# Kernel tuning notes

Measured on AMD Instinct MI355X. Metric: run time of the kernel, lower is better.

## Reference

```python
import jax, jax.numpy as jnp
import numpy as np
from jax import lax

NUM_HEADS = 4
EPS = 1e-12  # torch F.normalize eps


def _conv1x1(x, w):
    # x: [b, cin, h, w], w: [cout, cin] -> [b, cout, h, w]
    return jnp.einsum('bchw,oc->bohw', x, w)


def _dwconv3x3(x, w):
    # depthwise 3x3, padding=1; w: [C, 1, 3, 3]
    return lax.conv_general_dilated(
        x, w, window_strides=(1, 1), padding='SAME',
        feature_group_count=x.shape[1],
        dimension_numbers=('NCHW', 'OIHW', 'NCHW'))


def _l2norm(x):
    # F.normalize over last dim
    n = jnp.linalg.norm(x, axis=-1, keepdims=True)
    return x / jnp.maximum(n, EPS)


def _mdta(q, k, v, temperature, h, w):
    # q,k,v: [b, C, h, w] -> channel attention per head -> [b, C, h, w]
    b, c, _, _ = q.shape
    ch = c // NUM_HEADS
    def to_heads(t):
        return t.reshape(b, NUM_HEADS, ch, h * w)  # b head c (hw)
    qh, kh, vh = to_heads(q), to_heads(k), to_heads(v)
    qh = _l2norm(qh)
    kh = _l2norm(kh)
    attn = jnp.einsum('bhcn,bhdn->bhcd', qh, kh) * temperature  # [b,head,ch,ch]
    attn = jax.nn.softmax(attn, axis=-1)
    out = jnp.einsum('bhcd,bhdn->bhcn', attn, vh)
    return out.reshape(b, c, h, w)


def setup_inputs() -> dict:
    key = jax.random.key(0)
    ks = jax.random.split(key, 7)
    b, c, h, w = 2, 192, 128, 128
    return {
        'x': jax.random.normal(ks[0], (b, c, h, w), jnp.float32),
        'y': jax.random.normal(ks[1], (b, c, h, w), jnp.float32),
        'qkv_w': jax.random.normal(ks[2], (3 * c, c), jnp.float32) * (1.0 / np.sqrt(c)),
        'dw_w': jax.random.normal(ks[3], (3 * c, 1, 3, 3), jnp.float32) * (1.0 / 3.0),
        'kv_w': jax.random.normal(ks[4], (2 * c, c), jnp.float32) * (1.0 / np.sqrt(c)),
        'proj_w': jax.random.normal(ks[5], (c, c), jnp.float32) * (1.0 / np.sqrt(c)),
        'temperature': jnp.ones((NUM_HEADS, 1, 1), jnp.float32),
    }


def reference(x, y, qkv_w, dw_w, kv_w, proj_w, temperature):
    b, c, h, w = x.shape
    qkv = _dwconv3x3(_conv1x1(x, qkv_w), dw_w)
    q, k, v = jnp.split(qkv, 3, axis=1)
    # intra_fusion_attention(q, y): kv from y, channel attention with q
    kv = _conv1x1(y, kv_w)
    k2, v2 = jnp.split(kv, 2, axis=1)
    q = _mdta(q, k2, v2, temperature, h, w)
    out = _mdta(q, k, v, temperature, h, w)
    return _conv1x1(out, proj_w)
```

## Files before the change

### kernel.cpp

```cpp
#include <hip/hip_runtime.h>
#include <hip/hip_bf16.h>

#define HW 16384
#define IMGW 128
#define Bsz 2
#define Cc 192
#define NH 4
#define CH 48
static const size_t CP = (size_t)Cc * HW;

typedef __attribute__((ext_vector_type(4))) float f32x4;
typedef __attribute__((ext_vector_type(8))) short short8;
typedef __attribute__((ext_vector_type(8))) unsigned short bf16x8;
typedef __attribute__((ext_vector_type(4))) unsigned short bf16x4;

__device__ __forceinline__ unsigned short f2bf(float f) {
  __hip_bfloat16 h = __float2bfloat16(f);
  return *reinterpret_cast<unsigned short*>(&h);
}
__device__ __forceinline__ float bf2f(unsigned short u) {
  union { unsigned int i; float f; } v;
  v.i = (unsigned int)u << 16;
  return v.f;
}

#define NWQKV (576 * 192)
#define NWKV  (384 * 192)
__global__ __launch_bounds__(256) void cast_weights_kernel(
    const float* __restrict__ qkv_w, const float* __restrict__ kv_w,
    unsigned short* __restrict__ wqkv, unsigned short* __restrict__ wkv) {
  int i = blockIdx.x * 256 + threadIdx.x;
  if (i < NWQKV) wqkv[i] = f2bf(qkv_w[i]);
  else if (i < NWQKV + NWKV) wkv[i - NWQKV] = f2bf(kv_w[i - NWQKV]);
}

__global__ __launch_bounds__(256) void cast_xy_kernel(
    const float* __restrict__ x, const float* __restrict__ y,
    unsigned short* __restrict__ xt, unsigned short* __restrict__ yt) {
  const int z = blockIdx.z;
  const int b = z & 1;
  const float* in = (z >> 1) ? y : x;
  unsigned short* outt = (z >> 1) ? yt : xt;
  const int c0 = blockIdx.y * 8;
  const int hw = blockIdx.x * 256 + threadIdx.x;
  const float* ib = in + (size_t)b * CP;
  bf16x8 u;
  #pragma unroll
  for (int j = 0; j < 8; ++j)
    u[j] = f2bf(ib[(size_t)(c0 + j) * HW + hw]);
  *(bf16x8*)&outt[(size_t)b * CP + (size_t)hw * Cc + c0] = u;
}

#define BMH 128
#define BNO 64
#define BKC 64
#define PADK 72

template <int OUTBF16>
__global__ __launch_bounds__(256) void conv_mfma_kernel(
    const unsigned short* __restrict__ xt,
    const unsigned short* __restrict__ wb,
    void* __restrict__ outv, int Cout, size_t wstride) {
  __shared__ __align__(16) short As[BMH * PADK];
  __shared__ __align__(16) short Bs[BNO * PADK];
  const int b = blockIdx.z;
  const int hw0 = blockIdx.x * BMH;
  const int o0 = blockIdx.y * BNO;
  const int tid = threadIdx.x;
  const int lane = tid & 63, wid = tid >> 6;
  const int wm = wid & 1, wn = wid >> 1;
  const unsigned short* xtb = xt + (size_t)b * CP + (size_t)hw0 * Cc;
  const unsigned short* wbb = wb + (size_t)b * wstride + (size_t)o0 * Cc;
  f32x4 acc[4][2] = {};
  for (int k0 = 0; k0 < Cc; k0 += BKC) {
    #pragma unroll
    for (int p = 0; p < 4; ++p) {
      int i = tid + p * 256;
      int row = i >> 3, cc = i & 7;
      *(short8*)&As[row * PADK + cc * 8] =
          *(const short8*)(xtb + (size_t)row * Cc + k0 + cc * 8);
    }
    #pragma unroll
    for (int p = 0; p < 2; ++p) {
      int i = tid + p * 256;
      int row = i >> 3, cc = i & 7;
      *(short8*)&Bs[row * PADK + cc * 8] =
          *(const short8*)(wbb + (size_t)row * Cc + k0 + cc * 8);
    }
    __syncthreads();
    #pragma unroll
    for (int ks = 0; ks < 2; ++ks) {
      short8 bfrag[2];
      #pragma unroll
      for (int fn = 0; fn < 2; ++fn)
        bfrag[fn] = *(short8*)&Bs[(wn * 32 + fn * 16 + (lane & 15)) * PADK +
                                  ks * 32 + (lane >> 4) * 8];
      #pragma unroll
      for (int fm = 0; fm < 4; ++fm) {
        short8 afrag = *(short8*)&As[(wm * 64 + fm * 16 + (lane & 15)) * PADK +
                                     ks * 32 + (lane >> 4) * 8];
        #pragma unroll
        for (int fn = 0; fn < 2; ++fn)
          acc[fm][fn] = __builtin_amdgcn_mfma_f32_16x16x32_bf16(
              afrag, bfrag[fn], acc[fm][fn], 0, 0, 0);
      }
    }
    __syncthreads();
  }
  #pragma unroll
  for (int fm = 0; fm < 4; ++fm)
    #pragma unroll
    for (int fn = 0; fn < 2; ++fn) {
      int o = o0 + wn * 32 + fn * 16 + (lane & 15);
      int hw = hw0 + wm * 64 + fm * 16 + ((lane >> 4) << 2);
      if (OUTBF16) {
        bf16x4 u;
        #pragma unroll
        for (int r = 0; r < 4; ++r) u[r] = f2bf(acc[fm][fn][r]);
        *(bf16x4*)&((unsigned short*)outv)[((size_t)b * Cout + o) * HW + hw] = u;
      } else {
        *(f32x4*)&((float*)outv)[((size_t)b * Cout + o) * HW + hw] = acc[fm][fn];
      }
    }
}

__global__ __launch_bounds__(256) void dwconv_kernel(
    const unsigned short* __restrict__ in, const float* __restrict__ wgt,
    unsigned short* __restrict__ out, int Ctot) {
  const int b = blockIdx.z, ch = blockIdx.y;
  const int p0 = blockIdx.x * 2048 + threadIdx.x * 8;
  const int y = p0 >> 7, x0 = p0 & 127;
  const unsigned short* ip = in + ((size_t)b * Ctot + ch) * HW;
  const float* wp = wgt + ch * 9;
  float acc[8] = {};
  #pragma unroll
  for (int dy = -1; dy <= 1; ++dy) {
    int yy = y + dy;
    if (yy < 0 || yy > IMGW - 1) continue;
    const unsigned short* rp = ip + yy * IMGW;
    float r[10];
    bf16x8 mid = *(const bf16x8*)&rp[x0];
    #pragma unroll
    for (int e = 0; e < 8; ++e) r[e + 1] = bf2f(mid[e]);
    r[0] = (x0 > 0) ? bf2f(rp[x0 - 1]) : 0.f;
    r[9] = (x0 < 120) ? bf2f(rp[x0 + 8]) : 0.f;
    #pragma unroll
    for (int dx = 0; dx < 3; ++dx) {
      float wv = wp[(dy + 1) * 3 + dx];
      #pragma unroll
      for (int e = 0; e < 8; ++e) acc[e] += wv * r[e + dx];
    }
  }
  bf16x8 u;
  #pragma unroll
  for (int e = 0; e < 8; ++e) u[e] = f2bf(acc[e]);
  *(bf16x8*)&out[((size_t)b * Ctot + ch) * HW + p0] = u;
}

__global__ __launch_bounds__(256) void norm3_kernel(
    const unsigned short* __restrict__ qkvb,
    const unsigned short* __restrict__ kvb, float* __restrict__ inv) {
  const int kind = blockIdx.x / 384;
  const int row = blockIdx.x % 384;
  const int b = row / Cc, r = row % Cc;
  const unsigned short* p;
  if (kind == 0)      p = qkvb + (size_t)b * 3 * CP + (size_t)r * HW;
  else if (kind == 1) p = kvb + (size_t)b * 2 * CP + (size_t)r * HW;
  else                p = qkvb + (size_t)b * 3 * CP + CP + (size_t)r * HW;
  float s = 0.f;
  for (int i = threadIdx.x * 8; i < HW; i += 2048) {
    bf16x8 u = *(const bf16x8*)&p[i];
    #pragma unroll
    for (int j = 0; j < 8; ++j) {
      float v = bf2f(u[j]);
      s += v * v;
    }
  }
  #pragma unroll
  for (int off = 32; off; off >>= 1) s += __shfl_down(s, off);
  __shared__ float red[4];
  if ((threadIdx.x & 63) == 0) red[threadIdx.x >> 6] = s;
  __syncthreads();
  if (threadIdx.x == 0) {
    float t = red[0] + red[1] + red[2] + red[3];
    inv[blockIdx.x] = 1.f / fmaxf(sqrtf(t), 1e-12f);
  }
}

#define PK 136
#define NCHUNK 16
__global__ __launch_bounds__(256) void gram_mfma_kernel(
    const unsigned short* __restrict__ qkvb,
    const unsigned short* __restrict__ kvb, float* __restrict__ spart) {
  __shared__ __align__(16) char lds_raw[4 * 2304 * 4];
  short* Qs = (short*)lds_raw;
  short* Ks = Qs + 48 * PK;
  float* Rs = (float*)lds_raw;
  const int pair = blockIdx.z;
  const int bh = blockIdx.y, b = bh >> 2, hd = bh & 3;
  const int n0 = blockIdx.x * 1024;
  const int tid = threadIdx.x, lane = tid & 63, wid = tid >> 6;
  const unsigned short *ap, *bp;
  size_t as_, bs_;
  if (pair == 0)      { ap = qkvb;      as_ = 3 * CP; bp = kvb;       bs_ = 2 * CP; }
  else if (pair == 1) { ap = kvb + CP;  as_ = 2 * CP; bp = qkvb + CP; bs_ = 3 * CP; }
  else                { ap = kvb + CP;  as_ = 2 * CP; bp = kvb + CP;  bs_ = 2 * CP; }
  const unsigned short* qb = ap + (size_t)b * as_ + (size_t)(hd * CH) * HW + n0;
  const unsigned short* kb = bp + (size_t)b * bs_ + (size_t)(hd * CH) * HW + n0;
  f32x4 acc[3][3] = {};
  #pragma unroll 1
  for (int it = 0; it < 8; ++it) {
    #pragma unroll
    for (int p = 0; p < 3; ++p) {
      int c = tid + p * 256;
      int row = c >> 4, col = c & 15;
      *(short8*)&Qs[row * PK + col * 8] =
          *(const short8*)(qb + (size_t)row * HW + it * 128 + col * 8);
      *(short8*)&Ks[row * PK + col * 8] =
          *(const short8*)(kb + (size_t)row * HW + it * 128 + col * 8);
    }
    __syncthreads();
    short8 af[3], bfr[3];
    #pragma unroll
    for (int t = 0; t < 3; ++t) {
      af[t]  = *(short8*)&Qs[(t * 16 + (lane & 15)) * PK + wid * 32 + (lane >> 4) * 8];
      bfr[t] = *(short8*)&Ks[(t * 16 + (lane & 15)) * PK + wid * 32 + (lane >> 4) * 8];
    }
    #pragma unroll
    for (int mt = 0; mt < 3; ++mt)
      #pragma unroll
      for (int nt = 0; nt < 3; ++nt)
        acc[mt][nt] = __builtin_amdgcn_mfma_f32_16x16x32_bf16(
            af[mt], bfr[nt], acc[mt][nt], 0, 0, 0);
    __syncthreads();
  }
  #pragma unroll
  for (int mt = 0; mt < 3; ++mt)
    #pragma unroll
    for (int nt = 0; nt < 3; ++nt)
      #pragma unroll
      for (int r = 0; r < 4; ++r) {
        int i = mt * 16 + ((lane >> 4) << 2) + r;
        int j = nt * 16 + (lane & 15);
        Rs[wid * 2304 + i * 48 + j] = acc[mt][nt][r];
      }
  __syncthreads();
  float* sp = spart + ((size_t)(pair * 8 + bh) * NCHUNK + blockIdx.x) * 2304;
  for (int e = tid; e < 2304; e += 256)
    sp[e] = Rs[e] + Rs[2304 + e] + Rs[2 * 2304 + e] + Rs[3 * 2304 + e];
}

__global__ __launch_bounds__(256) void gram_reduce_kernel(
    const float* __restrict__ spart, float* __restrict__ G) {
  int idx = blockIdx.x * 256 + threadIdx.x;
  if (idx >= 3 * 8 * 2304) return;
  int pb = idx / 2304;
  int e = idx - pb * 2304;
  const float* sp = spart + (size_t)pb * NCHUNK * 2304 + e;
  float s = 0.f;
  #pragma unroll
  for (int c = 0; c < NCHUNK; ++c) s += sp[(size_t)c * 2304];
  G[idx] = s;
}

__global__ __launch_bounds__(256) void finalize_a2_kernel(
    const float* __restrict__ G, const float* __restrict__ inv,
    const float* __restrict__ temp, float* __restrict__ attn2) {
  __shared__ float A1[2304], GVV[2304], GVK[2304], S2[2304];
  __shared__ float invq1[48];
  const int bh = blockIdx.x, b = bh >> 2, hd = bh & 3;
  const int tid = threadIdx.x;
  const float tp = temp[hd];
  const float* invQ  = inv;
  const float* invK2 = inv + 384;
  const float* invK  = inv + 768;
  for (int e = tid; e < 2304; e += 256) {
    int i = e / 48, j = e - i * 48;
    A1[e] = G[(size_t)(0 * 8 + bh) * 2304 + e] *
            invQ[b * Cc + hd * CH + i] * invK2[b * Cc + hd * CH + j] * tp;
    GVV[e] = G[(size_t)(2 * 8 + bh) * 2304 + e];
    GVK[e] = G[(size_t)(1 * 8 + bh) * 2304 + e];
  }
  __syncthreads();
  if (tid < 192) {
    const int i = tid >> 2, g = tid & 3;
    float v[12];
    float m = -1e30f;
    #pragma unroll
    for (int k = 0; k < 12; ++k) {
      v[k] = A1[i * 48 + g * 12 + k];
      m = fmaxf(m, v[k]);
    }
    m = fmaxf(m, __shfl_xor(m, 1));
    m = fmaxf(m, __shfl_xor(m, 2));
    float sum = 0.f;
    #pragma unroll
    for (int k = 0; k < 12; ++k) {
      v[k] = expf(v[k] - m);
      sum += v[k];
    }
    sum += __shfl_xor(sum, 1);
    sum += __shfl_xor(sum, 2);
    float r = 1.f / sum;
    #pragma unroll
    for (int k = 0; k < 12; ++k) A1[i * 48 + g * 12 + k] = v[k] * r;
  }
  __syncthreads();
  const int ti = tid >> 4, tj = tid & 15;
  {
    float c[3][3] = {};
    #pragma unroll 4
    for (int d = 0; d < 48; ++d) {
      float a0 = A1[ti * 48 + d], a1 = A1[(ti + 16) * 48 + d],
            a2 = A1[(ti + 32) * 48 + d];
      float b0 = GVV[d * 48 + tj], b1 = GVV[d * 48 + tj + 16],
            b2 = GVV[d * 48 + tj + 32];
      c[0][0] += a0 * b0; c[0][1] += a0 * b1; c[0][2] += a0 * b2;
      c[1][0] += a1 * b0; c[1][1] += a1 * b1; c[1][2] += a1 * b2;
      c[2][0] += a2 * b0; c[2][1] += a2 * b1; c[2][2] += a2 * b2;
    }
    #pragma unroll
    for (int ii = 0; ii < 3; ++ii) {
      float p = 0.f;
      #pragma unroll
      for (int jj = 0; jj < 3; ++jj)
        p += c[ii][jj] * A1[(ti + 16 * ii) * 48 + tj + 16 * jj];
      p += __shfl_xor(p, 1);
      p += __shfl_xor(p, 2);
      p += __shfl_xor(p, 4);
      p += __shfl_xor(p, 8);
      if (tj == 0)
        invq1[ti + 16 * ii] = 1.f / fmaxf(sqrtf(fmaxf(p, 0.f)), 1e-12f);
    }
  }
  __syncthreads();
  {
    float s[3][3] = {};
    #pragma unroll 4
    for (int d = 0; d < 48; ++d) {
      float a0 = A1[ti * 48 + d], a1 = A1[(ti + 16) * 48 + d],
            a2 = A1[(ti + 32) * 48 + d];
      float b0 = GVK[d * 48 + tj], b1 = GVK[d * 48 + tj + 16],
            b2 = GVK[d * 48 + tj + 32];
      s[0][0] += a0 * b0; s[0][1] += a0 * b1; s[0][2] += a0 * b2;
      s[1][0] += a1 * b0; s[1][1] += a1 * b1; s[1][2] += a1 * b2;
      s[2][0] += a2 * b0; s[2][1] += a2 * b1; s[2][2] += a2 * b2;
    }
    #pragma unroll
    for (int ii = 0; ii < 3; ++ii)
      #pragma unroll
      for (int jj = 0; jj < 3; ++jj) {
        int i = ti + 16 * ii, j = tj + 16 * jj;
        S2[i * 48 + j] = s[ii][jj] * invq1[i] *
                         invK[b * Cc + hd * CH + j] * tp;
      }
  }
  __syncthreads();
  if (tid < 192) {
    const int i = tid >> 2, g = tid & 3;
    float v[12];
    float m = -1e30f;
    #pragma unroll
    for (int k = 0; k < 12; ++k) {
      v[k] = S2[i * 48 + g * 12 + k];
      m = fmaxf(m, v[k]);
    }
    m = fmaxf(m, __shfl_xor(m, 1));
    m = fmaxf(m, __shfl_xor(m, 2));
    float sum = 0.f;
    #pragma unroll
    for (int k = 0; k < 12; ++k) {
      v[k] = expf(v[k] - m);
      sum += v[k];
    }
    sum += __shfl_xor(sum, 1);
    sum += __shfl_xor(sum, 2);
    float r = 1.f / sum;
    #pragma unroll
    for (int k = 0; k < 12; ++k)
      attn2[(size_t)bh * 2304 + i * 48 + g * 12 + k] = v[k] * r;
  }
}

__global__ __launch_bounds__(192) void mproj_kernel(
    const float* __restrict__ P, const float* __restrict__ attn2,
    unsigned short* __restrict__ Mb) {
  const int b = blockIdx.y, o = blockIdx.x;
  const int c = threadIdx.x;
  const int hd = c / 48, j = c - hd * 48;
  const float* prow = P + (size_t)o * Cc + hd * 48;
  const float* arow = attn2 + (size_t)(b * 4 + hd) * 2304 + j;
  float s = 0.f;
  #pragma unroll 8
  for (int i = 0; i < 48; ++i) s += prow[i] * arow[(size_t)i * 48];
  Mb[((size_t)b * Cc + o) * Cc + c] = f2bf(s);
}

__global__ __launch_bounds__(256) void vtrans_kernel(
    const unsigned short* __restrict__ v, size_t vbs,
    unsigned short* __restrict__ vt) {
  __shared__ unsigned short LT[64 * 65];
  const int b = blockIdx.z;
  const int c0 = blockIdx.y * 64;
  const int h0 = blockIdx.x * 64;
  const int tid = threadIdx.x;
  const unsigned short* ip = v + (size_t)b * vbs + (size_t)c0 * HW + h0;
  #pragma unroll
  for (int e = 0; e < 2; ++e) {
    int idx = e * 256 + tid;
    int c = idx >> 3, hg = idx & 7;
    bf16x8 r = *(const bf16x8*)(ip + (size_t)c * HW + hg * 8);
    #pragma unroll
    for (int j = 0; j < 8; ++j) LT[c * 65 + hg * 8 + j] = r[j];
  }
  __syncthreads();
  unsigned short* op = vt + (size_t)b * CP + (size_t)h0 * Cc + c0;
  #pragma unroll
  for (int e = 0; e < 2; ++e) {
    int idx = e * 256 + tid;
    int hw = idx >> 3, cg = idx & 7;
    bf16x8 u;
    #pragma unroll
    for (int j = 0; j < 8; ++j) u[j] = LT[(cg * 8 + j) * 65 + hw];
    *(bf16x8*)&op[(size_t)hw * Cc + cg * 8] = u;
  }
}

extern "C" void kernel_launch(void* const* d_in, const int* in_sizes, int n_in,
                              void* d_out, int out_size, void* d_ws, size_t ws_size,
                              hipStream_t stream) {
  const float* x      = (const float*)d_in[0];
  const float* y      = (const float*)d_in[1];
  const float* qkv_w  = (const float*)d_in[2];
  const float* dw_w   = (const float*)d_in[3];
  const float* kv_w   = (const float*)d_in[4];
  const float* proj_w = (const float*)d_in[5];
  const float* temp   = (const float*)d_in[6];
  float* out = (float*)d_out;
  float* ws  = (float*)d_ws;

  const size_t SF = (size_t)Bsz * CP;
  unsigned short* qkvb   = (unsigned short*)ws;
  unsigned short* kvb    = (unsigned short*)(ws + 3 * SF / 2);
  unsigned short* qkvpre = (unsigned short*)(ws + 5 * SF / 2);
  unsigned short* xt     = (unsigned short*)(ws + 4 * SF);
  unsigned short* vt     = xt;
  unsigned short* yt     = (unsigned short*)(ws + 9 * SF / 2);
  float* inv   = ws + 5 * SF;
  float* spart = inv + 1152;
  float* G     = spart + (size_t)3 * 8 * NCHUNK * 2304;
  float* attn2 = G + 3 * 8 * 2304;
  unsigned short* Mb   = (unsigned short*)(attn2 + 8 * 2304);
  unsigned short* wqkv = Mb + (size_t)Bsz * Cc * Cc;
  unsigned short* wkv  = wqkv + NWQKV;

  dim3 blk(256);

  cast_weights_kernel<<<dim3((NWQKV + NWKV + 255) / 256), blk, 0, stream>>>(
      qkv_w, kv_w, wqkv, wkv);
  cast_xy_kernel<<<dim3(HW / 256, Cc / 8, 2 * Bsz), blk, 0, stream>>>(
      x, y, xt, yt);

  conv_mfma_kernel<1><<<dim3(HW / BMH, 576 / BNO, Bsz), blk, 0, stream>>>(
      xt, wqkv, qkvpre, 3 * Cc, 0);
  dwconv_kernel<<<dim3(HW / 2048, 3 * Cc, Bsz), blk, 0, stream>>>(
      qkvpre, dw_w, qkvb, 3 * Cc);
  conv_mfma_kernel<1><<<dim3(HW / BMH, 384 / BNO, Bsz), blk, 0, stream>>>(
      yt, wkv, kvb, 2 * Cc, 0);

  norm3_kernel<<<dim3(3 * 384), blk, 0, stream>>>(qkvb, kvb, inv);

  gram_mfma_kernel<<<dim3(NCHUNK, 8, 3), blk, 0, stream>>>(qkvb, kvb, spart);
  gram_reduce_kernel<<<dim3(216), blk, 0, stream>>>(spart, G);

  finalize_a2_kernel<<<dim3(8), blk, 0, stream>>>(G, inv, temp, attn2);
  mproj_kernel<<<dim3(Cc, Bsz), dim3(192), 0, stream>>>(proj_w, attn2, Mb);

  vtrans_kernel<<<dim3(HW / 64, Cc / 64, Bsz), blk, 0, stream>>>(
      qkvb + 2 * CP, 3 * CP, vt);
  conv_mfma_kernel<0><<<dim3(HW / BMH, Cc / BNO, Bsz), blk, 0, stream>>>(
      vt, Mb, out, Cc, (size_t)Cc * Cc);
}
```

Baseline: 132.3 us.

## Fuse input cast/transpose into 1x1 conv GEMM and keep full-K A tile resident

The separate fp32-to-bf16 transpose kernel for x/y and the v-transpose kernel are removed. The conv GEMM now reads channel-major inputs directly, converting and transposing them into a 64-pixel x 192-channel LDS tile. That tile stays resident while the block loops over all output-channel tiles, reloading only the weights. This removes extra global round-trips and launches, but the grid shrinks to 256 wide blocks with fewer MFMAs per weight load and higher LDS use.

Result: faster. 117.3 us (median of 2 runs) (-11.3%).

```diff
diff --git a/kernel.cpp b/kernel.cpp
--- a/kernel.cpp
+++ b/kernel.cpp
@@ -34,70 +34,75 @@
   else if (i < NWQKV + NWKV) wkv[i - NWQKV] = f2bf(kv_w[i - NWQKV]);
 }
 
-__global__ __launch_bounds__(256) void cast_xy_kernel(
-    const float* __restrict__ x, const float* __restrict__ y,
-    unsigned short* __restrict__ xt, unsigned short* __restrict__ yt) {
-  const int z = blockIdx.z;
-  const int b = z & 1;
-  const float* in = (z >> 1) ? y : x;
-  unsigned short* outt = (z >> 1) ? yt : xt;
-  const int c0 = blockIdx.y * 8;
-  const int hw = blockIdx.x * 256 + threadIdx.x;
-  const float* ib = in + (size_t)b * CP;
-  bf16x8 u;
-  #pragma unroll
-  for (int j = 0; j < 8; ++j)
-    u[j] = f2bf(ib[(size_t)(c0 + j) * HW + hw]);
-  *(bf16x8*)&outt[(size_t)b * CP + (size_t)hw * Cc + c0] = u;
-}
-
-#define BMH 128
-#define BNO 64
-#define BKC 64
-#define PADK 72
-
-template <int OUTBF16>
+#define APAD 200
+
+template <int INKIND, int OUTBF16>
 __global__ __launch_bounds__(256) void conv_mfma_kernel(
-    const unsigned short* __restrict__ xt,
-    const unsigned short* __restrict__ wb,
-    void* __restrict__ outv, int Cout, size_t wstride) {
-  __shared__ __align__(16) short As[BMH * PADK];
-  __shared__ __align__(16) short Bs[BNO * PADK];
+    const void* __restrict__ src, size_t src_bstride,
+    const unsigned short* __restrict__ wb, size_t wstride,
+    void* __restrict__ outv, int Cout) {
+  __shared__ __align__(16) short As[64 * APAD];
+  __shared__ __align__(16) short Bs[64 * APAD];
+  unsigned int* As32 = (unsigned int*)As;
   const int b = blockIdx.z;
-  const int hw0 = blockIdx.x * BMH;
-  const int o0 = blockIdx.y * BNO;
+  const int hw0 = blockIdx.x * 64;
   const int tid = threadIdx.x;
   const int lane = tid & 63, wid = tid >> 6;
   const int wm = wid & 1, wn = wid >> 1;
-  const unsigned short* xtb = xt + (size_t)b * CP + (size_t)hw0 * Cc;
-  const unsigned short* wbb = wb + (size_t)b * wstride + (size_t)o0 * Cc;
-  f32x4 acc[4][2] = {};
-  for (int k0 = 0; k0 < Cc; k0 += BKC) {
-    #pragma unroll
-    for (int p = 0; p < 4; ++p) {
+  const int l = tid & 15, pp0 = tid >> 4;
+  const unsigned short* wbbase = wb + (size_t)b * wstride;
+  const int NT = Cout >> 6;
+
+  #pragma unroll
+  for (int kp = 0; kp < 3; ++kp) {
+    #pragma unroll
+    for (int it = 0; it < 2; ++it) {
+      int pp = pp0 + 16 * it;
+      int c0 = kp * 64 + 2 * pp;
+      if (INKIND == 1) {
+        const float* r0 = (const float*)src + (size_t)b * src_bstride +
+                          (size_t)c0 * HW + hw0 + l * 4;
+        f32x4 v0 = *(const f32x4*)r0;
+        f32x4 v1 = *(const f32x4*)(r0 + HW);
+        #pragma unroll
+        for (int i = 0; i < 4; ++i)
+          As32[(l * 4 + i) * (APAD / 2) + kp * 32 + pp] =
+              (unsigned int)f2bf(v0[i]) | ((unsigned int)f2bf(v1[i]) << 16);
+      } else {
+        const unsigned short* r0 = (const unsigned short*)src +
+                                   (size_t)b * src_bstride +
+                                   (size_t)c0 * HW + hw0 + l * 4;
+        bf16x4 v0 = *(const bf16x4*)r0;
+        bf16x4 v1 = *(const bf16x4*)(r0 + HW);
+        #pragma unroll
+        for (int i = 0; i < 4; ++i)
+          As32[(l * 4 + i) * (APAD / 2) + kp * 32 + pp] =
+              (unsigned int)v0[i] | ((unsigned int)v1[i] << 16);
+      }
+    }
+  }
+
+  for (int ot = 0; ot < NT; ++ot) {
+    const unsigned short* wbb = wbbase + (size_t)(ot * 64) * Cc;
+    #pragma unroll
+    for (int p = 0; p < 6; ++p) {
       int i = tid + p * 256;
-      int row = i >> 3, cc = i & 7;
-      *(short8*)&As[row * PADK + cc * 8] =
-          *(const short8*)(xtb + (size_t)row * Cc + k0 + cc * 8);
-    }
-    #pragma unroll
-    for (int p = 0; p < 2; ++p) {
-      int i = tid + p * 256;
-      int row = i >> 3, cc = i & 7;
-      *(short8*)&Bs[row * PADK + cc * 8] =
-          *(const short8*)(wbb + (size_t)row * Cc + k0 + cc * 8);
+      int row = i / 24, cc = i - (i / 24) * 24;
+      *(short8*)&Bs[row * APAD + cc * 8] =
+          *(const short8*)(wbb + (size_t)row * Cc + cc * 8);
     }
     __syncthreads();
-    #pragma unroll
-    for (int ks = 0; ks < 2; ++ks) {
+    f32x4 acc[2][2] = {};
+    #pragma unroll
+    for (int ks = 0; ks < 6; ++ks) {
       short8 bfrag[2];
       #pragma unroll
       for (int fn = 0; fn < 2; ++fn)
-        bfrag[fn] = *(short8*)&Bs[(wn * 32 + fn * 16 + (lane & 15)) * PADK +
+        bfrag[fn] = *(short8*)&Bs[(wn * 32 + fn * 16 + (lane & 15)) * APAD +
                                   ks * 32 + (lane >> 4) * 8];
       #pragma unroll
-      for (int fm = 0; fm < 4; ++fm) {
-        short8 afrag = *(short8*)&As[(wm * 64 + fm * 16 + (lane & 15)) * PADK +
+      for (int fm = 0; fm < 2; ++fm) {
+        short8 afrag = *(short8*)&As[(wm * 32 + fm * 16 + (lane & 15)) * APAD +
                                      ks * 32 + (lane >> 4) * 8];
         #pragma unroll
         for (int fn = 0; fn < 2; ++fn)
@@ -106,22 +111,22 @@
       }
     }
     __syncthreads();
-  }
-  #pragma unroll
-  for (int fm = 0; fm < 4; ++fm)
-    #pragma unroll
-    for (int fn = 0; fn < 2; ++fn) {
-      int o = o0 + wn * 32 + fn * 16 + (lane & 15);
-      int hw = hw0 + wm * 64 + fm * 16 + ((lane >> 4) << 2);
-      if (OUTBF16) {
-        bf16x4 u;
-        #pragma unroll
-        for (int r = 0; r < 4; ++r) u[r] = f2bf(acc[fm][fn][r]);
-        *(bf16x4*)&((unsigned short*)outv)[((size_t)b * Cout + o) * HW + hw] = u;
-      } else {
-        *(f32x4*)&((float*)outv)[((size_t)b * Cout + o) * HW + hw] = acc[fm][fn];
+    #pragma unroll
+    for (int fm = 0; fm < 2; ++fm)
+      #pragma unroll
+      for (int fn = 0; fn < 2; ++fn) {
+        int o = ot * 64 + wn * 32 + fn * 16 + (lane & 15);
+        int hw = hw0 + wm * 32 + fm * 16 + ((lane >> 4) << 2);
+        if (OUTBF16) {
+          bf16x4 u;
+          #pragma unroll
+          for (int r = 0; r < 4; ++r) u[r] = f2bf(acc[fm][fn][r]);
+          *(bf16x4*)&((unsigned short*)outv)[((size_t)b * Cout + o) * HW + hw] = u;
+        } else {
+          *(f32x4*)&((float*)outv)[((size_t)b * Cout + o) * HW + hw] = acc[fm][fn];
+        }
       }
-    }
+  }
 }
 
 __global__ __launch_bounds__(256) void dwconv_kernel(
@@ -396,36 +401,6 @@
   Mb[((size_t)b * Cc + o) * Cc + c] = f2bf(s);
 }
 
-__global__ __launch_bounds__(256) void vtrans_kernel(
-    const unsigned short* __restrict__ v, size_t vbs,
-    unsigned short* __restrict__ vt) {
-  __shared__ unsigned short LT[64 * 65];
-  const int b = blockIdx.z;
-  const int c0 = blockIdx.y * 64;
-  const int h0 = blockIdx.x * 64;
-  const int tid = threadIdx.x;
-  const unsigned short* ip = v + (size_t)b * vbs + (size_t)c0 * HW + h0;
-  #pragma unroll
-  for (int e = 0; e < 2; ++e) {
-    int idx = e * 256 + tid;
-    int c = idx >> 3, hg = idx & 7;
-    bf16x8 r = *(const bf16x8*)(ip + (size_t)c * HW + hg * 8);
-    #pragma unroll
-    for (int j = 0; j < 8; ++j) LT[c * 65 + hg * 8 + j] = r[j];
-  }
-  __syncthreads();
-  unsigned short* op = vt + (size_t)b * CP + (size_t)h0 * Cc + c0;
-  #pragma unroll
-  for (int e = 0; e < 2; ++e) {
-    int idx = e * 256 + tid;
-    int hw = idx >> 3, cg = idx & 7;
-    bf16x8 u;
-    #pragma unroll
-    for (int j = 0; j < 8; ++j) u[j] = LT[(cg * 8 + j) * 65 + hw];
-    *(bf16x8*)&op[(size_t)hw * Cc + cg * 8] = u;
-  }
-}
-
 extern "C" void kernel_launch(void* const* d_in, const int* in_sizes, int n_in,
                               void* d_out, int out_size, void* d_ws, size_t ws_size,
                               hipStream_t stream) {
@@ -443,10 +418,7 @@
   unsigned short* qkvb   = (unsigned short*)ws;
   unsigned short* kvb    = (unsigned short*)(ws + 3 * SF / 2);
   unsigned short* qkvpre = (unsigned short*)(ws + 5 * SF / 2);
-  unsigned short* xt     = (unsigned short*)(ws + 4 * SF);
-  unsigned short* vt     = xt;
-  unsigned short* yt     = (unsigned short*)(ws + 9 * SF / 2);
-  float* inv   = ws + 5 * SF;
+  float* inv   = ws + 4 * SF;
   float* spart = inv + 1152;
   float* G     = spart + (size_t)3 * 8 * NCHUNK * 2304;
   float* attn2 = G + 3 * 8 * 2304;
@@ -458,15 +430,13 @@
 
   cast_weights_kernel<<<dim3((NWQKV + NWKV + 255) / 256), blk, 0, stream>>>(
       qkv_w, kv_w, wqkv, wkv);
-  cast_xy_kernel<<<dim3(HW / 256, Cc / 8, 2 * Bsz), blk, 0, stream>>>(
-      x, y, xt, yt);
-
-  conv_mfma_kernel<1><<<dim3(HW / BMH, 576 / BNO, Bsz), blk, 0, stream>>>(
-      xt, wqkv, qkvpre, 3 * Cc, 0);
+
+  conv_mfma_kernel<1, 1><<<dim3(HW / 64, 1, Bsz), blk, 0, stream>>>(
+      x, CP, wqkv, 0, qkvpre, 3 * Cc);
   dwconv_kernel<<<dim3(HW / 2048, 3 * Cc, Bsz), blk, 0, stream>>>(
       qkvpre, dw_w, qkvb, 3 * Cc);
-  conv_mfma_kernel<1><<<dim3(HW / BMH, 384 / BNO, Bsz), blk, 0, stream>>>(
-      yt, wkv, kvb, 2 * Cc, 0);
+  conv_mfma_kernel<1, 1><<<dim3(HW / 64, 1, Bsz), blk, 0, stream>>>(
+      y, CP, wkv, 0, kvb, 2 * Cc);
 
   norm3_kernel<<<dim3(3 * 384), blk, 0, stream>>>(qkvb, kvb, inv);
 
@@ -476,8 +446,6 @@
   finalize_a2_kernel<<<dim3(8), blk, 0, stream>>>(G, inv, temp, attn2);
   mproj_kernel<<<dim3(Cc, Bsz), dim3(192), 0, stream>>>(proj_w, attn2, Mb);
 
-  vtrans_kernel<<<dim3(HW / 64, Cc / 64, Bsz), blk, 0, stream>>>(
-      qkvb + 2 * CP, 3 * CP, vt);
-  conv_mfma_kernel<0><<<dim3(HW / BMH, Cc / BNO, Bsz), blk, 0, stream>>>(
-      vt, Mb, out, Cc, (size_t)Cc * Cc);
-}
+  conv_mfma_kernel<2, 0><<<dim3(HW / 64, 1, Bsz), blk, 0, stream>>>(
+      qkvb + 2 * CP, 3 * CP, Mb, (size_t)Cc * Cc, out, Cc);
+}
```
